# Optimization experiments

Hardware: AMD Instinct MI355X
Metric: run time of the kernel (lower is better)

The kernel has to match this reference:

```python
import jax, jax.numpy as jnp
import numpy as np

B = 4096      # batch
D = 64        # state_dim
H = 512       # hidden_dim


def setup_inputs() -> dict:
    key = jax.random.key(0)
    ks = jax.random.split(key, 16)

    def init(k, shape, fan_in):
        return jax.random.normal(k, shape, dtype=jnp.float32) / np.float32(np.sqrt(fan_in))

    mu = jax.random.normal(ks[0], (B, D), dtype=jnp.float32)
    sigma_diag = 0.1 * jax.random.uniform(ks[1], (B, D), dtype=jnp.float32) + 0.01
    states = jnp.concatenate([mu, sigma_diag], axis=1)  # [B, 2D]

    return {
        "t": jnp.float32(0.5),
        "states": states,
        # dynamics net: tanh MLP D -> H -> H -> D
        "W1": init(ks[2], (H, D), D), "b1": jnp.zeros((H,), jnp.float32),
        "W2": init(ks[3], (H, H), H), "b2": jnp.zeros((H,), jnp.float32),
        "W3": init(ks[4], (D, H), H), "b3": jnp.zeros((D,), jnp.float32),
        # process-noise net: tanh MLP D -> H -> H -> D, softplus head (diagonal Q)
        "V1": init(ks[5], (H, D), D), "c1": jnp.zeros((H,), jnp.float32),
        "V2": init(ks[6], (H, H), H), "c2": jnp.zeros((H,), jnp.float32),
        "V3": init(ks[7], (D, H), H), "c3": jnp.zeros((D,), jnp.float32),
    }


def reference(t, states, W1, b1, W2, b2, W3, b3, V1, c1, V2, c2, V3, c3):
    # UPN ODE function, diagonal-covariance path.
    mu = states[:, :D]          # [B, D]
    sigma_diag = states[:, D:]  # [B, D]

    # dynamics MLP forward (t is an autonomous-system placeholder, unused)
    h1 = jnp.tanh(mu @ W1.T + b1)   # [B, H]
    h2 = jnp.tanh(h1 @ W2.T + b2)   # [B, H]
    mu_drift = h2 @ W3.T + b3       # [B, D]

    # analytic batched Jacobian of the tanh MLP: J = W3 diag(1-h2^2) W2 diag(1-h1^2) W1
    d1 = 1.0 - h1 * h1              # [B, H]
    d2 = 1.0 - h2 * h2              # [B, H]
    inner = jnp.einsum('hk,bk,kd->bhd', W2, d1, W1)   # [B, H, D]
    J = jnp.einsum('oh,bh,bhd->bod', W3, d2, inner)   # [B, D, D]
    J_diag = jnp.diagonal(J, axis1=1, axis2=2)        # [B, D]

    # process-noise net: diagonal Q, softplus ensures positivity
    g1 = jnp.tanh(mu @ V1.T + c1)
    g2 = jnp.tanh(g1 @ V2.T + c2)
    Q_diag = jax.nn.softplus(g2 @ V3.T + c3)          # [B, D]

    sigma_drift = 2.0 * J_diag * sigma_diag + Q_diag  # [B, D]
    return jnp.concatenate([mu_drift, sigma_drift], axis=1)  # [B, 2D]
```

## Files before the change

kernel.cpp:

```cpp
#include <hip/hip_runtime.h>
#include <hip/hip_bf16.h>

#define BB 4096
#define DD 64
#define HH 512

typedef __hip_bfloat16 bf16;
typedef _Float16 f16;
typedef __attribute__((ext_vector_type(8))) short bf16x8;
typedef __attribute__((ext_vector_type(8))) _Float16 f16x8;
typedef __attribute__((ext_vector_type(4))) float f32x4;

__device__ __forceinline__ float bf2f(bf16 x) { return __bfloat162float(x); }
__device__ __forceinline__ float u16tof(unsigned short u) {
  union { unsigned int i; float f; } v; v.i = ((unsigned int)u) << 16; return v.f;
}
#define BC8(p) __builtin_bit_cast(bf16x8, *(const uint4*)(p))
#define BCH8(p) __builtin_bit_cast(f16x8, *(const uint4*)(p))

__device__ __forceinline__ void gl16(const void* g, void* l) {
  __builtin_amdgcn_global_load_lds((__attribute__((address_space(1))) void*)g,
                                   (__attribute__((address_space(3))) void*)l,
                                   16, 0, 0);
}


__global__ __launch_bounds__(256) void cvt_weights(
    const float* __restrict__ W2, const float* __restrict__ V2,
    const float* __restrict__ W1, const float* __restrict__ V1,
    const float* __restrict__ W3, const float* __restrict__ V3,
    bf16* __restrict__ W2bf, bf16* __restrict__ V2bf,
    bf16* __restrict__ W1bf, bf16* __restrict__ V1bf,
    bf16* __restrict__ W3bf, bf16* __restrict__ V3bf,
    f16* __restrict__ W2sw, f16* __restrict__ W1sw) {
  int blk = blockIdx.x, t = threadIdx.x;
  if (blk < 512) {
    const float* src = (blk < 256) ? W2 : V2;
    bf16* dst = (blk < 256) ? W2bf : V2bf;
    int i = ((blk & 255) * 256 + t) * 4;
    float4 v = *(const float4*)(src + i);
    bf16 o[4] = {__float2bfloat16(v.x), __float2bfloat16(v.y),
                 __float2bfloat16(v.z), __float2bfloat16(v.w)};
    *(uint2*)(dst + i) = *(uint2*)o;
  } else if (blk < 640) {
    int uid = (blk - 512) * 256 + t;
    int kc = uid >> 12, rem = uid & 4095;
    int h = rem >> 3, u = rem & 7;
    const float* src = W2 + (size_t)h * HH + kc * 64 + u * 8;
    float4 a = *(const float4*)src;
    float4 b = *(const float4*)(src + 4);
    f16 o[8] = {(f16)a.x, (f16)a.y, (f16)a.z, (f16)a.w,
                (f16)b.x, (f16)b.y, (f16)b.z, (f16)b.w};
    *(uint4*)(W2sw + (size_t)((kc * 512 + h) * 8 + (u ^ (h & 7))) * 8) = *(uint4*)o;
  } else if (blk < 656) {
    int uid = (blk - 640) * 256 + t;
    int kc = uid >> 9, rem = uid & 511;
    int dl = rem >> 3, u = rem & 7;
    f16 o[8];
#pragma unroll
    for (int e = 0; e < 8; ++e)
      o[e] = (f16)W1[(size_t)(kc * 64 + u * 8 + e) * DD + dl];
    *(uint4*)(W1sw + (size_t)((kc * 64 + dl) * 8 + (u ^ (dl & 7))) * 8) = *(uint4*)o;
  } else {
    int which = (blk - 656) >> 5;
    int local = (blk - 656) & 31;
    const float* src = (which == 0) ? W1 : (which == 1) ? V1 : (which == 2) ? W3 : V3;
    bf16* dst = (which == 0) ? W1bf : (which == 1) ? V1bf : (which == 2) ? W3bf : V3bf;
    int i = (local * 256 + t) * 4;
    float4 v = *(const float4*)(src + i);
    bf16 o[4] = {__float2bfloat16(v.x), __float2bfloat16(v.y),
                 __float2bfloat16(v.z), __float2bfloat16(v.w)};
    *(uint2*)(dst + i) = *(uint2*)o;
  }
}

__global__ __launch_bounds__(256) void fwd(
    const float* __restrict__ states,
    const bf16* __restrict__ W1bf, const float* __restrict__ b1,
    const bf16* __restrict__ W2bf, const float* __restrict__ b2,
    const bf16* __restrict__ W3bf, const float* __restrict__ b3,
    const bf16* __restrict__ V1bf, const float* __restrict__ c1,
    const bf16* __restrict__ V2bf, const float* __restrict__ c2,
    const bf16* __restrict__ V3bf, const float* __restrict__ c3,
    bf16* __restrict__ Xbf, bf16* __restrict__ Ybf, float* __restrict__ out) {
  __shared__ __align__(16) bf16 mus[16 * 72];
  __shared__ __align__(16) bf16 Xres[16 * 520];
  __shared__ __align__(16) bf16 Bs[128 * 72];
  __shared__ __align__(16) bf16 Ych[16 * 136];
  const int bt = blockIdx.x * 16;
  const int path = blockIdx.y;
  const bf16* Wa = path ? V1bf : W1bf;
  const float* ba = path ? c1 : b1;
  const bf16* Wb = path ? V2bf : W2bf;
  const float* bbv = path ? c2 : b2;
  const bf16* Wc = path ? V3bf : W3bf;
  const float* bcv = path ? c3 : b3;
  const int t = threadIdx.x;
  const int lane = t & 63;
  const int w = t >> 6;
  const int c = lane & 15, q = lane >> 4;

  if (t < 128) {
    int row = t >> 3, cg = (t & 7) * 8;
    bf16 o[8];
#pragma unroll
    for (int j = 0; j < 8; j += 4) {
      float4 v = *(const float4*)(states + (size_t)(bt + row) * 128 + cg + j);
      o[j] = __float2bfloat16(v.x); o[j + 1] = __float2bfloat16(v.y);
      o[j + 2] = __float2bfloat16(v.z); o[j + 3] = __float2bfloat16(v.w);
    }
    *(uint4*)(mus + row * 72 + cg) = *(const uint4*)o;
  }
  __syncthreads();

  for (int nch = 0; nch < 4; ++nch) {
    if (nch) __syncthreads();
#pragma unroll
    for (int i = 0; i < 4; ++i) {
      int g = t + i * 256;
      int row = g >> 3, kb = (g & 7) * 8;
      *(uint4*)(Bs + row * 72 + kb) =
          *(const uint4*)(Wa + (size_t)(nch * 128 + row) * 64 + kb);
    }
    __syncthreads();
    f32x4 acc1[2] = {};
#pragma unroll
    for (int s = 0; s < 2; ++s) {
      bf16x8 af = BC8(mus + c * 72 + s * 32 + q * 8);
#pragma unroll
      for (int nt = 0; nt < 2; ++nt) {
        bf16x8 bfr = BC8(Bs + (w * 32 + nt * 16 + c) * 72 + s * 32 + q * 8);
        acc1[nt] = __builtin_amdgcn_mfma_f32_16x16x32_bf16(af, bfr, acc1[nt], 0, 0, 0);
      }
    }
#pragma unroll
    for (int nt = 0; nt < 2; ++nt) {
      int col = nch * 128 + w * 32 + nt * 16 + c;
      float bias = ba[col];
#pragma unroll
      for (int r = 0; r < 4; ++r) {
        int row = q * 4 + r;
        float x = tanhf(acc1[nt][r] + bias);
        Xres[row * 520 + col] = __float2bfloat16(x);
        if (!path) Xbf[(size_t)(bt + row) * HH + col] = __float2bfloat16(x);
      }
    }
  }
  __syncthreads();

  f32x4 acc3 = {};
  for (int hch = 0; hch < 4; ++hch) {
    f32x4 acc2[2] = {};
    for (int kc = 0; kc < 8; ++kc) {
      __syncthreads();
#pragma unroll
      for (int i = 0; i < 4; ++i) {
        int g = t + i * 256;
        int row = g >> 3, kb = (g & 7) * 8;
        *(uint4*)(Bs + row * 72 + kb) =
            *(const uint4*)(Wb + (size_t)(hch * 128 + row) * HH + kc * 64 + kb);
      }
      __syncthreads();
#pragma unroll
      for (int s = 0; s < 2; ++s) {
        bf16x8 af = BC8(Xres + c * 520 + kc * 64 + s * 32 + q * 8);
#pragma unroll
        for (int nt = 0; nt < 2; ++nt) {
          bf16x8 bfr = BC8(Bs + (w * 32 + nt * 16 + c) * 72 + s * 32 + q * 8);
          acc2[nt] = __builtin_amdgcn_mfma_f32_16x16x32_bf16(af, bfr, acc2[nt], 0, 0, 0);
        }
      }
    }
    __syncthreads();
#pragma unroll
    for (int nt = 0; nt < 2; ++nt) {
      int hl = w * 32 + nt * 16 + c;
      int h = hch * 128 + hl;
      float bias = bbv[h];
#pragma unroll
      for (int r = 0; r < 4; ++r) {
        int row = q * 4 + r;
        float y = tanhf(acc2[nt][r] + bias);
        Ych[row * 136 + hl] = __float2bfloat16(y);
        if (!path) Ybf[(size_t)(bt + row) * HH + h] = __float2bfloat16(y);
      }
    }
    __syncthreads();
#pragma unroll
    for (int s3 = 0; s3 < 4; ++s3) {
      bf16x8 bf3 = BC8(Wc + (size_t)(w * 16 + c) * HH + hch * 128 + s3 * 32 + q * 8);
      bf16x8 af3 = BC8(Ych + c * 136 + s3 * 32 + q * 8);
      acc3 = __builtin_amdgcn_mfma_f32_16x16x32_bf16(af3, bf3, acc3, 0, 0, 0);
    }
  }
  {
    int o = w * 16 + c;
    float bias = bcv[o];
#pragma unroll
    for (int r = 0; r < 4; ++r) {
      int row = q * 4 + r;
      float v = acc3[r] + bias;
      if (path) {
        v = fmaxf(v, 0.0f) + log1pf(expf(-fabsf(v)));
        out[(size_t)(bt + row) * 128 + 64 + o] = v;
      } else {
        out[(size_t)(bt + row) * 128 + o] = v;
      }
    }
  }
}

#define LDSB(buf) ((buf) * 32768)
#define LDSA(buf) (98304 + (buf) * 8192)
#define LDSD1 122880
#define LDSD2 126976
#define LDSRED 98304

#define STAGE(kc_, buf_) do {                                                  \
    const char* gb_ = (const char*)W2sw + ((size_t)(kc_) * 512 + h0) * 128;    \
    char* lb_ = (char*)lds + LDSB(buf_);                                       \
    gl16(gb_ + t * 16, lb_ + t * 16);                                          \
    gl16(gb_ + 8192 + t * 16, lb_ + 8192 + t * 16);                            \
    gl16(gb_ + 16384 + t * 16, lb_ + 16384 + t * 16);                          \
    gl16(gb_ + 24576 + t * 16, lb_ + 24576 + t * 16);                          \
    gl16((const char*)W1sw + (kc_) * 8192 + t * 16,                            \
         (char*)lds + LDSA(buf_) + t * 16);                                    \
  } while (0)

__global__ __launch_bounds__(512, 2) void k4_gemm(
    const bf16* __restrict__ Xbf, const bf16* __restrict__ Ybf,
    const f16* __restrict__ W1sw, const f16* __restrict__ W2sw,
    const float* __restrict__ W3, float* __restrict__ Jpart) {
  __shared__ __align__(16) char lds[131072];
  const int bt = blockIdx.x;
  const int h0 = blockIdx.y * 256;
  const int t = threadIdx.x;
  const int lane = t & 63;
  const int w = t >> 6;
  const int c = lane & 15, q = lane >> 4;
  const int wr = w >> 2, wc = w & 3;
  const int b0 = bt * 4;

  {
    int e = t * 4, j = e >> 9, k = e & 511;
    ushort4 xv = *(const ushort4*)((const unsigned short*)Xbf +
                                   (size_t)(b0 + j) * HH + k);
    f16 o[4];
    float x;
    x = u16tof(xv.x); o[0] = (f16)(1.f - x * x);
    x = u16tof(xv.y); o[1] = (f16)(1.f - x * x);
    x = u16tof(xv.z); o[2] = (f16)(1.f - x * x);
    x = u16tof(xv.w); o[3] = (f16)(1.f - x * x);
    *(uint2*)(lds + LDSD1 + e * 2) = *(uint2*)o;
  }
  {
    int e = t * 2, j = e >> 8, n = e & 255;
    ushort2 yv = *(const ushort2*)((const unsigned short*)Ybf +
                                   (size_t)(b0 + j) * HH + h0 + n);
    float y0 = u16tof(yv.x), y1 = u16tof(yv.y);
    float2 d2v = {1.f - y0 * y0, 1.f - y1 * y1};
    *(float2*)(lds + LDSD2 + e * 4) = d2v;
  }
  __syncthreads();

  STAGE(0, 0);
  STAGE(1, 1);

  const int cj = c & 7;
  const int j16_0 = ((0 + q) ^ cj) * 16;
  const int j16_1 = ((4 + q) ^ cj) * 16;
  const int arow = c * 128;
  const int brow = (wc * 64 + c) * 128;
  const int d1base = LDSD1 + wr * 2048 + q * 16;

  f32x4 acc[8][4] = {};

#pragma unroll
  for (int kc = 0; kc < 8; ++kc) {
    const int buf = kc % 3;
    if (kc < 7) { asm volatile("s_waitcnt vmcnt(5)\n\ts_barrier" ::: "memory"); }
    else        { asm volatile("s_waitcnt vmcnt(0)\n\ts_barrier" ::: "memory"); }
    if (kc < 6) STAGE(kc + 2, (kc + 2) % 3);

    f16x8 bfr[4][2], w1f[4][2], d1v[2][2];
#pragma unroll
    for (int nt = 0; nt < 4; ++nt) {
      bfr[nt][0] = BCH8(lds + LDSB(buf) + brow + nt * 2048 + j16_0);
      bfr[nt][1] = BCH8(lds + LDSB(buf) + brow + nt * 2048 + j16_1);
    }
#pragma unroll
    for (int i = 0; i < 4; ++i) {
      w1f[i][0] = BCH8(lds + LDSA(buf) + arow + i * 2048 + j16_0);
      w1f[i][1] = BCH8(lds + LDSA(buf) + arow + i * 2048 + j16_1);
    }
#pragma unroll
    for (int b = 0; b < 2; ++b) {
      d1v[b][0] = BCH8(lds + d1base + b * 1024 + kc * 128);
      d1v[b][1] = BCH8(lds + d1base + b * 1024 + kc * 128 + 64);
    }
    __builtin_amdgcn_s_setprio(1);
#pragma unroll
    for (int mt = 0; mt < 8; ++mt) {
#pragma unroll
      for (int s = 0; s < 2; ++s) {
        f16x8 av = w1f[mt & 3][s] * d1v[mt >> 2][s];
#pragma unroll
        for (int nt = 0; nt < 4; ++nt)
          acc[mt][nt] = __builtin_amdgcn_mfma_f32_16x16x32_f16(
              av, bfr[nt][s], acc[mt][nt], 0, 0, 0);
      }
    }
    __builtin_amdgcn_s_setprio(0);
  }
  __syncthreads();

#pragma unroll
  for (int i = 0; i < 8; ++i) {
    int e = (t + i * 512) * 4;
    int dl = e >> 8, col = e & 255;
    float4 v = *(const float4*)(W3 + (size_t)dl * HH + h0 + col);
    *(float*)(lds + ((col + 0) * 72 + dl) * 4) = v.x;
    *(float*)(lds + ((col + 1) * 72 + dl) * 4) = v.y;
    *(float*)(lds + ((col + 2) * 72 + dl) * 4) = v.z;
    *(float*)(lds + ((col + 3) * 72 + dl) * 4) = v.w;
  }
  __syncthreads();

  float d2r[2][4];
#pragma unroll
  for (int bh = 0; bh < 2; ++bh)
#pragma unroll
    for (int nt = 0; nt < 4; ++nt)
      d2r[bh][nt] = *(const float*)(
          lds + LDSD2 + ((wr * 2 + bh) * 256 + wc * 64 + nt * 16 + c) * 4);

  float vsum[8][4] = {};
#pragma unroll
  for (int mt4 = 0; mt4 < 4; ++mt4)
#pragma unroll
    for (int nt = 0; nt < 4; ++nt) {
      f32x4 w3v = *(const f32x4*)(
          lds + ((wc * 64 + nt * 16 + c) * 72 + mt4 * 16 + q * 4) * 4);
#pragma unroll
      for (int bh = 0; bh < 2; ++bh) {
        const int mt = bh * 4 + mt4;
        float sc = d2r[bh][nt];
#pragma unroll
        for (int r = 0; r < 4; ++r)
          vsum[mt][r] += acc[mt][nt][r] * w3v[r] * sc;
      }
    }

#pragma unroll
  for (int mt = 0; mt < 8; ++mt)
#pragma unroll
    for (int r = 0; r < 4; ++r) {
      float v = vsum[mt][r];
      v += __shfl_xor(v, 1);
      v += __shfl_xor(v, 2);
      v += __shfl_xor(v, 4);
      v += __shfl_xor(v, 8);
      if (c == 0)
        *(float*)(lds + LDSRED +
                  (wc * 256 + wr * 128 + mt * 16 + q * 4 + r) * 4) = v;
    }
  __syncthreads();
  if (t < 256) {
    float J = *(const float*)(lds + LDSRED + t * 4) +
              *(const float*)(lds + LDSRED + (256 + t) * 4) +
              *(const float*)(lds + LDSRED + (512 + t) * 4) +
              *(const float*)(lds + LDSRED + (768 + t) * 4);
    Jpart[(size_t)blockIdx.y * (BB * 64) + (size_t)bt * 256 + t] = J;
  }
}

__global__ __launch_bounds__(256) void combine(
    const float* __restrict__ Jpart, const float* __restrict__ states,
    float* __restrict__ out) {
  int idx = blockIdx.x * 256 + threadIdx.x;
  int b = idx >> 6, d = idx & 63;
  const int plane = BB * 64;
  float J = Jpart[idx] + Jpart[plane + idx];
  float sig = states[(size_t)b * 128 + 64 + d];
  float qd = out[(size_t)b * 128 + 64 + d];
  out[(size_t)b * 128 + 64 + d] = 2.0f * J * sig + qd;
}

extern "C" void kernel_launch(void* const* d_in, const int* in_sizes, int n_in,
                              void* d_out, int out_size, void* d_ws, size_t ws_size,
                              hipStream_t stream) {
  const float* states = (const float*)d_in[1];
  const float* W1 = (const float*)d_in[2];
  const float* b1 = (const float*)d_in[3];
  const float* W2 = (const float*)d_in[4];
  const float* b2 = (const float*)d_in[5];
  const float* W3 = (const float*)d_in[6];
  const float* b3 = (const float*)d_in[7];
  const float* V1 = (const float*)d_in[8];
  const float* c1 = (const float*)d_in[9];
  const float* V2 = (const float*)d_in[10];
  const float* c2 = (const float*)d_in[11];
  const float* V3 = (const float*)d_in[12];
  const float* c3 = (const float*)d_in[13];
  float* out = (float*)d_out;

  bf16* Xbf = (bf16*)d_ws;
  bf16* Ybf = Xbf + (size_t)BB * HH;
  bf16* W2bf = Ybf + (size_t)BB * HH;
  bf16* V2bf = W2bf + (size_t)HH * HH;
  bf16* W1bf = V2bf + (size_t)HH * HH;
  bf16* V1bf = W1bf + (size_t)HH * DD;
  bf16* W3bf = V1bf + (size_t)HH * DD;
  bf16* V3bf = W3bf + (size_t)DD * HH;
  f16* W1sw = (f16*)(V3bf + (size_t)DD * HH);
  f16* W2sw = W1sw + (size_t)DD * HH;
  float* Jpart = (float*)(W2sw + (size_t)HH * HH);

  cvt_weights<<<dim3(784), 256, 0, stream>>>(W2, V2, W1, V1, W3, V3,
                                             W2bf, V2bf, W1bf, V1bf,
                                             W3bf, V3bf, W2sw, W1sw);
  fwd<<<dim3(256, 2), 256, 0, stream>>>(states, W1bf, b1, W2bf, b2, W3bf, b3,
                                        V1bf, c1, V2bf, c2, V3bf, c3,
                                        Xbf, Ybf, out);
  k4_gemm<<<dim3(1024, 2), 512, 0, stream>>>(Xbf, Ybf, W1sw, W2sw, W3, Jpart);
  combine<<<dim3(1024), 256, 0, stream>>>(Jpart, states, out);
}
```

Measured before the change: 320.8 us.

## Split GEMM k-step into four barrier-synchronized MFMA phases with interleaved prefetch

Restructures the k4_gemm main loop so each k-chunk runs in four sub-phases. Each phase loads a smaller set of LDS fragments, issues part of the next global-to-LDS prefetch, and then does a 16-MFMA group, with barriers between phases to keep waves in lockstep. This is meant to cut register pressure and spread memory traffic across the compute work. Separately, W3 is pre-transposed into a W3T buffer in cvt_weights, so the epilogue can fill LDS with float4 stores instead of scattered scalar stores. The cost is many more barriers per iteration and one extra conversion pass.

```diff
diff --git a/kernel.cpp b/kernel.cpp
--- a/kernel.cpp
+++ b/kernel.cpp
@@ -23,6 +23,10 @@
                                    (__attribute__((address_space(3))) void*)l,
                                    16, 0, 0);
 }
+
+#define BARRIER() __builtin_amdgcn_s_barrier()
+#define LGKM0() do { asm volatile("s_waitcnt lgkmcnt(0)" ::: "memory"); \
+                     __builtin_amdgcn_sched_barrier(0); } while (0)
 
 
 __global__ __launch_bounds__(256) void cvt_weights(
@@ -32,7 +36,7 @@
     bf16* __restrict__ W2bf, bf16* __restrict__ V2bf,
     bf16* __restrict__ W1bf, bf16* __restrict__ V1bf,
     bf16* __restrict__ W3bf, bf16* __restrict__ V3bf,
-    f16* __restrict__ W2sw, f16* __restrict__ W1sw) {
+    f16* __restrict__ W2sw, f16* __restrict__ W1sw, float* __restrict__ W3T) {
   int blk = blockIdx.x, t = threadIdx.x;
   if (blk < 512) {
     const float* src = (blk < 256) ? W2 : V2;
@@ -61,7 +65,7 @@
     for (int e = 0; e < 8; ++e)
       o[e] = (f16)W1[(size_t)(kc * 64 + u * 8 + e) * DD + dl];
     *(uint4*)(W1sw + (size_t)((kc * 64 + dl) * 8 + (u ^ (dl & 7))) * 8) = *(uint4*)o;
-  } else {
+  } else if (blk < 784) {
     int which = (blk - 656) >> 5;
     int local = (blk - 656) & 31;
     const float* src = (which == 0) ? W1 : (which == 1) ? V1 : (which == 2) ? W3 : V3;
@@ -71,6 +75,13 @@
     bf16 o[4] = {__float2bfloat16(v.x), __float2bfloat16(v.y),
                  __float2bfloat16(v.z), __float2bfloat16(v.w)};
     *(uint2*)(dst + i) = *(uint2*)o;
+  } else {
+    int e = ((blk - 784) * 256 + t) * 4;
+    int h = e >> 6, o0 = e & 63;
+    float o[4];
+#pragma unroll
+    for (int j = 0; j < 4; ++j) o[j] = W3[(size_t)(o0 + j) * HH + h];
+    *(float4*)(W3T + (size_t)h * 64 + o0) = *(float4*)o;
   }
 }
 
@@ -230,7 +241,7 @@
 __global__ __launch_bounds__(512, 2) void k4_gemm(
     const bf16* __restrict__ Xbf, const bf16* __restrict__ Ybf,
     const f16* __restrict__ W1sw, const f16* __restrict__ W2sw,
-    const float* __restrict__ W3, float* __restrict__ Jpart) {
+    const float* __restrict__ W3T, float* __restrict__ Jpart) {
   __shared__ __align__(16) char lds[131072];
   const int bt = blockIdx.x;
   const int h0 = blockIdx.y * 256;
@@ -265,64 +276,117 @@
 
   STAGE(0, 0);
   STAGE(1, 1);
+  asm volatile("s_waitcnt vmcnt(5)" ::: "memory");
+  BARRIER();
 
   const int cj = c & 7;
   const int j16_0 = ((0 + q) ^ cj) * 16;
   const int j16_1 = ((4 + q) ^ cj) * 16;
   const int arow = c * 128;
   const int brow = (wc * 64 + c) * 128;
-  const int d1base = LDSD1 + wr * 2048 + q * 16;
+  const char* d1b = (const char*)lds + LDSD1 + wr * 2048 + q * 16;
 
   f32x4 acc[8][4] = {};
 
 #pragma unroll
   for (int kc = 0; kc < 8; ++kc) {
-    const int buf = kc % 3;
-    if (kc < 7) { asm volatile("s_waitcnt vmcnt(5)\n\ts_barrier" ::: "memory"); }
-    else        { asm volatile("s_waitcnt vmcnt(0)\n\ts_barrier" ::: "memory"); }
-    if (kc < 6) STAGE(kc + 2, (kc + 2) % 3);
-
-    f16x8 bfr[4][2], w1f[4][2], d1v[2][2];
-#pragma unroll
-    for (int nt = 0; nt < 4; ++nt) {
-      bfr[nt][0] = BCH8(lds + LDSB(buf) + brow + nt * 2048 + j16_0);
-      bfr[nt][1] = BCH8(lds + LDSB(buf) + brow + nt * 2048 + j16_1);
-    }
-#pragma unroll
-    for (int i = 0; i < 4; ++i) {
-      w1f[i][0] = BCH8(lds + LDSA(buf) + arow + i * 2048 + j16_0);
-      w1f[i][1] = BCH8(lds + LDSA(buf) + arow + i * 2048 + j16_1);
-    }
-#pragma unroll
-    for (int b = 0; b < 2; ++b) {
-      d1v[b][0] = BCH8(lds + d1base + b * 1024 + kc * 128);
-      d1v[b][1] = BCH8(lds + d1base + b * 1024 + kc * 128 + 64);
-    }
+    const char* Bb = (const char*)lds + LDSB(kc % 3);
+    const char* Ab = (const char*)lds + LDSA(kc % 3);
+    const char* gB2 = (const char*)W2sw + ((size_t)(kc + 2) * 512 + h0) * 128;
+    const char* gA2 = (const char*)W1sw + (size_t)(kc + 2) * 8192;
+    char* lB2 = (char*)lds + LDSB((kc + 2) % 3);
+    char* lA2 = (char*)lds + LDSA((kc + 2) % 3);
+    f16x8 av;
+
+    f16x8 b0[4], a0[4];
+    f16x8 d00 = BCH8(d1b + kc * 128);
+#pragma unroll
+    for (int nt = 0; nt < 4; ++nt) b0[nt] = BCH8(Bb + brow + nt * 2048 + j16_0);
+#pragma unroll
+    for (int i = 0; i < 4; ++i) a0[i] = BCH8(Ab + arow + i * 2048 + j16_0);
+    if (kc < 6) {
+      gl16(gB2 + t * 16, lB2 + t * 16);
+      gl16(gB2 + 8192 + t * 16, lB2 + 8192 + t * 16);
+    }
+    BARRIER(); LGKM0();
     __builtin_amdgcn_s_setprio(1);
 #pragma unroll
-    for (int mt = 0; mt < 8; ++mt) {
-#pragma unroll
-      for (int s = 0; s < 2; ++s) {
-        f16x8 av = w1f[mt & 3][s] * d1v[mt >> 2][s];
-#pragma unroll
-        for (int nt = 0; nt < 4; ++nt)
-          acc[mt][nt] = __builtin_amdgcn_mfma_f32_16x16x32_f16(
-              av, bfr[nt][s], acc[mt][nt], 0, 0, 0);
-      }
+    for (int mt = 0; mt < 4; ++mt) {
+      av = a0[mt] * d00;
+#pragma unroll
+      for (int nt = 0; nt < 4; ++nt)
+        acc[mt][nt] = __builtin_amdgcn_mfma_f32_16x16x32_f16(
+            av, b0[nt], acc[mt][nt], 0, 0, 0);
     }
     __builtin_amdgcn_s_setprio(0);
+    BARRIER();
+
+    f16x8 d10 = BCH8(d1b + 1024 + kc * 128);
+    if (kc < 6) {
+      gl16(gB2 + 16384 + t * 16, lB2 + 16384 + t * 16);
+      gl16(gB2 + 24576 + t * 16, lB2 + 24576 + t * 16);
+    }
+    BARRIER(); LGKM0();
+    __builtin_amdgcn_s_setprio(1);
+#pragma unroll
+    for (int mt = 0; mt < 4; ++mt) {
+      av = a0[mt] * d10;
+#pragma unroll
+      for (int nt = 0; nt < 4; ++nt)
+        acc[mt + 4][nt] = __builtin_amdgcn_mfma_f32_16x16x32_f16(
+            av, b0[nt], acc[mt + 4][nt], 0, 0, 0);
+    }
+    __builtin_amdgcn_s_setprio(0);
+    BARRIER();
+
+    f16x8 b1[4], a1[4];
+    f16x8 d01 = BCH8(d1b + 64 + kc * 128);
+#pragma unroll
+    for (int nt = 0; nt < 4; ++nt) b1[nt] = BCH8(Bb + brow + nt * 2048 + j16_1);
+#pragma unroll
+    for (int i = 0; i < 4; ++i) a1[i] = BCH8(Ab + arow + i * 2048 + j16_1);
+    if (kc < 6) gl16(gA2 + t * 16, lA2 + t * 16);
+    BARRIER(); LGKM0();
+    __builtin_amdgcn_s_setprio(1);
+#pragma unroll
+    for (int mt = 0; mt < 4; ++mt) {
+      av = a1[mt] * d01;
+#pragma unroll
+      for (int nt = 0; nt < 4; ++nt)
+        acc[mt][nt] = __builtin_amdgcn_mfma_f32_16x16x32_f16(
+            av, b1[nt], acc[mt][nt], 0, 0, 0);
+    }
+    __builtin_amdgcn_s_setprio(0);
+    BARRIER();
+
+    f16x8 d11 = BCH8(d1b + 1024 + 64 + kc * 128);
+    BARRIER(); LGKM0();
+    __builtin_amdgcn_s_setprio(1);
+#pragma unroll
+    for (int mt = 0; mt < 4; ++mt) {
+      av = a1[mt] * d11;
+#pragma unroll
+      for (int nt = 0; nt < 4; ++nt)
+        acc[mt + 4][nt] = __builtin_amdgcn_mfma_f32_16x16x32_f16(
+            av, b1[nt], acc[mt + 4][nt], 0, 0, 0);
+    }
+    __builtin_amdgcn_s_setprio(0);
+    if (kc < 6) {
+      asm volatile("s_waitcnt vmcnt(5)" ::: "memory");
+      BARRIER();
+    } else if (kc == 6) {
+      asm volatile("s_waitcnt vmcnt(0)" ::: "memory");
+      BARRIER();
+    }
   }
   __syncthreads();
 
 #pragma unroll
   for (int i = 0; i < 8; ++i) {
     int e = (t + i * 512) * 4;
-    int dl = e >> 8, col = e & 255;
-    float4 v = *(const float4*)(W3 + (size_t)dl * HH + h0 + col);
-    *(float*)(lds + ((col + 0) * 72 + dl) * 4) = v.x;
-    *(float*)(lds + ((col + 1) * 72 + dl) * 4) = v.y;
-    *(float*)(lds + ((col + 2) * 72 + dl) * 4) = v.z;
-    *(float*)(lds + ((col + 3) * 72 + dl) * 4) = v.w;
+    int col = e >> 6, dl0 = e & 63;
+    float4 v = *(const float4*)(W3T + (size_t)(h0 + col) * 64 + dl0);
+    *(float4*)(lds + (col * 72 + dl0) * 4) = v;
   }
   __syncthreads();
 
@@ -414,14 +478,15 @@
   bf16* V3bf = W3bf + (size_t)DD * HH;
   f16* W1sw = (f16*)(V3bf + (size_t)DD * HH);
   f16* W2sw = W1sw + (size_t)DD * HH;
-  float* Jpart = (float*)(W2sw + (size_t)HH * HH);
-
-  cvt_weights<<<dim3(784), 256, 0, stream>>>(W2, V2, W1, V1, W3, V3,
+  float* W3T = (float*)(W2sw + (size_t)HH * HH);
+  float* Jpart = W3T + (size_t)HH * DD;
+
+  cvt_weights<<<dim3(816), 256, 0, stream>>>(W2, V2, W1, V1, W3, V3,
                                              W2bf, V2bf, W1bf, V1bf,
-                                             W3bf, V3bf, W2sw, W1sw);
+                                             W3bf, V3bf, W2sw, W1sw, W3T);
   fwd<<<dim3(256, 2), 256, 0, stream>>>(states, W1bf, b1, W2bf, b2, W3bf, b3,
                                         V1bf, c1, V2bf, c2, V3bf, c3,
                                         Xbf, Ybf, out);
-  k4_gemm<<<dim3(1024, 2), 512, 0, stream>>>(Xbf, Ybf, W1sw, W2sw, W3, Jpart);
+  k4_gemm<<<dim3(1024, 2), 512, 0, stream>>>(Xbf, Ybf, W1sw, W2sw, W3T, Jpart);
   combine<<<dim3(1024), 256, 0, stream>>>(Jpart, states, out);
 }
```

Result: faster. 281.7 us (-12.2%).
